# Kernel tuning notes

Hardware: AMD Instinct MI355X
Metric: run time of the kernel (lower is better)

Reference implementation:

```python
import jax
import jax.numpy as jnp
from jax import lax
import numpy as np

B, C, H, W = 16, 96, 112, 112
HIDDEN = 4 * C
LN_EPS = 1e-6  # ConvNeXt LayerNorm eps


def setup_inputs() -> dict:
    key = jax.random.key(0)
    ks = jax.random.split(key, 8)
    x = jax.random.normal(ks[0], (B, C, H, W), dtype=jnp.float32)
    # depthwise 7x7 kernel, HWIO with feature_group_count=C -> (7,7,1,C)
    dw_w = jax.random.normal(ks[1], (7, 7, 1, C), dtype=jnp.float32) * 0.02
    dw_b = jnp.zeros((C,), dtype=jnp.float32)
    gamma = jnp.ones((C,), dtype=jnp.float32)
    beta = jnp.zeros((C,), dtype=jnp.float32)
    w1 = jax.random.normal(ks[2], (C, HIDDEN), dtype=jnp.float32) * 0.02
    b1 = jnp.zeros((HIDDEN,), dtype=jnp.float32)
    w2 = jax.random.normal(ks[3], (HIDDEN, C), dtype=jnp.float32) * 0.02
    b2 = jnp.zeros((C,), dtype=jnp.float32)
    scale = jnp.full((C,), 1e-6, dtype=jnp.float32)  # block_scale init 1e-6
    return {"x": x, "dw_w": dw_w, "dw_b": dw_b, "gamma": gamma, "beta": beta,
            "w1": w1, "b1": b1, "w2": w2, "b2": b2, "scale": scale}


def reference(x, dw_w, dw_b, gamma, beta, w1, b1, w2, b2, scale):
    # depthwise 7x7, stride 1, padding 3 (SAME), groups = C
    y = lax.conv_general_dilated(
        x, dw_w, window_strides=(1, 1), padding="SAME",
        dimension_numbers=("NCHW", "HWIO", "NCHW"),
        feature_group_count=C,
    ) + dw_b[None, :, None, None]
    # BCHW -> BHWC
    y = jnp.transpose(y, (0, 2, 3, 1))
    # LayerNorm over channel dim
    mu = jnp.mean(y, axis=-1, keepdims=True)
    var = jnp.var(y, axis=-1, keepdims=True)
    y = (y - mu) * lax.rsqrt(var + LN_EPS) * gamma + beta
    # pointwise MLP with exact GELU (torch nn.GELU default)
    h = jax.nn.gelu(jnp.einsum("bhwc,cd->bhwd", y, w1) + b1, approximate=False)
    y = jnp.einsum("bhwd,dc->bhwc", h, w2) + b2
    # BHWC -> BCHW, scale, residual (eval mode: stochastic depth = identity)
    y = jnp.transpose(y, (0, 3, 1, 2))
    return scale[None, :, None, None] * y + x
```

## Files before the change

### kernel.cpp

```cpp
#include <hip/hip_runtime.h>
#include <hip/hip_bf16.h>

#define BATCH 16
#define CCH 96
#define HH 112
#define WW 112
#define HID 384
#define NPIX (BATCH * HH * WW)
#define HW (HH * WW)

#define PXB 128
#define ZROWD 50
#define SLICE_B 12288
#define RING_SLOTS 3
#define ZR_BYTES (PXB * ZROWD * 4)
#define B1_OFF (RING_SLOTS * SLICE_B)
#define SMEM_TOTAL (B1_OFF + 1536)

typedef __attribute__((ext_vector_type(8))) short bf16x8;
typedef __attribute__((ext_vector_type(4))) float f32x4;
typedef __attribute__((ext_vector_type(2))) float f32x2;
typedef __attribute__((ext_vector_type(4))) unsigned int uint4v;

typedef const __attribute__((address_space(1))) void gvoid_t;
typedef __attribute__((address_space(3))) void svoid_t;

__device__ __forceinline__ short f2bf(float v) {
    __hip_bfloat16 h = __float2bfloat16(v);
    return __builtin_bit_cast(short, h);
}
__device__ __forceinline__ float bf2f(short s) {
    unsigned int u = ((unsigned int)(unsigned short)s) << 16;
    return __builtin_bit_cast(float, u);
}
__device__ __forceinline__ float gelu_fast(float v) {
    float e = __expf(-1.702f * v);
    return v * __builtin_amdgcn_rcpf(1.0f + e);
}

__global__ __launch_bounds__(256) void pack_w(const float* __restrict__ w1,
                                              const float* __restrict__ w2,
                                              const float* __restrict__ gamma,
                                              const float* __restrict__ scale,
                                              short* __restrict__ wp) {
    int o = blockIdx.x * 256 + threadIdx.x;
    if (o >= 12 * 12 * 64 * 8) return;
    const int j   = o & 7;
    const int l   = (o >> 3) & 63;
    const int g   = o >> 9;
    const int f   = g % 12;
    const int kk2 = g / 12;
    float v;
    if (f < 6) {
        const int kk = f >> 1, mh = f & 1;
        const int c  = kk * 32 + (l >> 4) * 8 + j;
        const int d  = (2 * kk2 + mh) * 16 + (l & 15);
        v = gamma[c] * w1[c * HID + d];
    } else {
        const int nt2 = f - 6;
        const int dd  = kk2 * 32 + ((j >> 2) << 4) + ((l >> 4) << 2) + (j & 3);
        const int n   = nt2 * 16 + (l & 15);
        v = w2[dd * CCH + n] * scale[n];
    }
    wp[o] = f2bf(v);
}

__global__ __launch_bounds__(256) void pack_bias(const float* __restrict__ w1,
                                                 const float* __restrict__ b1,
                                                 const float* __restrict__ beta,
                                                 const float* __restrict__ b2,
                                                 const float* __restrict__ scale,
                                                 float* __restrict__ b1p,
                                                 float* __restrict__ b2p) {
    int t = blockIdx.x * 256 + threadIdx.x;
    if (t < HID) {
        float s = b1[t];
        for (int c = 0; c < CCH; ++c) s += beta[c] * w1[c * HID + t];
        b1p[t] = s;
    } else if (t < HID + CCH) {
        int c = t - HID;
        b2p[c] = scale[c] * b2[c];
    }
}

__global__ __launch_bounds__(256) void conv_kernel(
    const float* __restrict__ x, const float* __restrict__ dww,
    const float* __restrict__ dwb, short* __restrict__ y)
{
    __shared__ float xs[34][128];

    const int t = threadIdx.x;
    const int p = blockIdx.x;
    int o = (p & 7) * 768 + (p >> 3);
    const int ht = o & 3;  o >>= 2;
    const int c  = o % CCH;
    const int b  = o / CCH;
    const int h0 = ht * 28;
    const float* xc = x + (size_t)(b * CCH + c) * HW;

    float4 vbuf[5];
    #pragma unroll
    for (int k = 0; k < 5; ++k) {
        const int idx = t + 256 * k;
        const int r  = idx >> 5;
        const int j  = idx & 31;
        const int gh = h0 - 3 + r;
        float4 v = make_float4(0.f, 0.f, 0.f, 0.f);
        if (idx < 1088 && (unsigned)gh < HH && j >= 1 && j <= 28)
            v = *reinterpret_cast<const float4*>(xc + gh * WW + 4 * j - 4);
        vbuf[k] = v;
    }
    #pragma unroll
    for (int k = 0; k < 5; ++k) {
        const int idx = t + 256 * k;
        if (idx < 1088)
            *reinterpret_cast<float4*>(&xs[0][0] + (idx >> 5) * 128 + (idx & 31) * 4) = vbuf[k];
    }
    __syncthreads();

    const int col = t & 127;
    const int rg  = t >> 7;
    if (col < WW) {
        const int r0 = rg * 14;
        const float bias = dwb[c];
        f32x2 accp[7];
        #pragma unroll
        for (int r = 0; r < 7; ++r) accp[r] = (f32x2){bias, bias};
        #pragma unroll
        for (int kw = 0; kw < 7; ++kw) {
            float cv[20];
            #pragma unroll
            for (int i = 0; i < 20; ++i) cv[i] = xs[r0 + i][col + kw + 1];
            #pragma unroll
            for (int kh = 0; kh < 7; ++kh) {
                const float wt = dww[(kh * 7 + kw) * CCH + c];
                const f32x2 wt2 = (f32x2){wt, wt};
                #pragma unroll
                for (int r = 0; r < 7; ++r) {
                    f32x2 v;
                    v.x = cv[2 * r + kh];
                    v.y = cv[2 * r + kh + 1];
                    accp[r] += v * wt2;
                }
            }
        }
        short* yc = y + (size_t)(b * CCH + c) * HW + (h0 + r0) * WW + col;
        #pragma unroll
        for (int r = 0; r < 7; ++r) {
            yc[(2 * r) * WW]     = f2bf(accp[r].x);
            yc[(2 * r + 1) * WW] = f2bf(accp[r].y);
        }
    }
}

__global__ __launch_bounds__(256, 4) void mlp_kernel(
    const short* __restrict__ ybuf, const char* __restrict__ wp,
    const float* __restrict__ b1p, const float* __restrict__ b2p,
    const float* __restrict__ x, float* __restrict__ out)
{
    __shared__ __align__(16) char smem[SMEM_TOTAL];
    unsigned int* zr = (unsigned int*)smem;
    float* b1l = (float*)(smem + B1_OFF);

    const int t    = threadIdx.x;
    const int lane = t & 63;
    const int wv   = t >> 6;
    const int l15  = lane & 15;
    const int q    = lane >> 4;
    const int px0  = blockIdx.x * PXB;
    const int b    = px0 / HW;
    const int hw0  = px0 - b * HW;

    if (t < 192) {
        const int pq = t / 48;
        const int cp = t - pq * 48;
        const unsigned int* Ap = (const unsigned int*)(ybuf +
            (size_t)(b * CCH + 2 * cp) * HW + hw0 + pq * 32);
        const unsigned int* Bp = (const unsigned int*)(ybuf +
            (size_t)(b * CCH + 2 * cp + 1) * HW + hw0 + pq * 32);
        #pragma unroll
        for (int e = 0; e < 4; ++e) {
            const uint4v A  = *reinterpret_cast<const uint4v*>(Ap + e * 4);
            const uint4v Bv = *reinterpret_cast<const uint4v*>(Bp + e * 4);
            #pragma unroll
            for (int k = 0; k < 4; ++k) {
                const int px = pq * 32 + e * 8 + 2 * k;
                zr[px * ZROWD + cp]       = (A[k] & 0xffffu) | (Bv[k] << 16);
                zr[(px + 1) * ZROWD + cp] = (A[k] >> 16) | (Bv[k] & 0xffff0000u);
            }
        }
    } else {
        const int i0 = (t - 192) * 6;
        #pragma unroll
        for (int i2 = 0; i2 < 6; ++i2) b1l[i0 + i2] = b1p[i0 + i2];
    }

    f32x4 acc2[2][6];
    #pragma unroll
    for (int nt2 = 0; nt2 < 6; ++nt2) {
        const int c = nt2 * 16 + l15;
        const float bv = b2p[c];
        #pragma unroll
        for (int m2 = 0; m2 < 2; ++m2) {
            const size_t g = (size_t)(b * CCH + c) * HW + hw0 + wv * 32 + m2 * 16 + q * 4;
            const f32x4 xv = *reinterpret_cast<const f32x4*>(x + g);
            acc2[m2][nt2].x = bv + xv.x;  acc2[m2][nt2].y = bv + xv.y;
            acc2[m2][nt2].z = bv + xv.z;  acc2[m2][nt2].w = bv + xv.w;
        }
    }
    __syncthreads();

    bf16x8 za[2][3];
    #pragma unroll
    for (int nt = 0; nt < 2; ++nt) {
        const int row = wv * 32 + nt * 16 + l15;
        const char* base = smem + row * (ZROWD * 4) + q * 16;
        float s1 = 0.f, s2 = 0.f;
        #pragma unroll
        for (int kk = 0; kk < 3; ++kk) {
            za[nt][kk] = *reinterpret_cast<const bf16x8*>(base + kk * 64);
            #pragma unroll
            for (int j = 0; j < 8; ++j) {
                const float v = bf2f(za[nt][kk][j]);
                s1 += v; s2 += v * v;
            }
        }
        s1 += __shfl_xor(s1, 16, 64);  s2 += __shfl_xor(s2, 16, 64);
        s1 += __shfl_xor(s1, 32, 64);  s2 += __shfl_xor(s2, 32, 64);
        const float mu   = s1 * (1.0f / CCH);
        const float rstd = rsqrtf(s2 * (1.0f / CCH) - mu * mu + 1e-6f);
        #pragma unroll
        for (int kk = 0; kk < 3; ++kk)
            #pragma unroll
            for (int j = 0; j < 8; ++j)
                za[nt][kk][j] = f2bf((bf2f(za[nt][kk][j]) - mu) * rstd);
    }
    __syncthreads();

    asm volatile("s_waitcnt vmcnt(0)" ::: "memory");

    #define STAGE_F(SL, SLOT)                                                       \
        {                                                                           \
            const char* _s = wp + (size_t)(SL) * SLICE_B + (wv * 3) * 1024 +        \
                             lane * 16;                                             \
            char* _d = smem + (SLOT) * SLICE_B + (wv * 3) * 1024;                   \
            __builtin_amdgcn_global_load_lds((gvoid_t*)(_s),        (svoid_t*)(_d),        16, 0, 0); \
            __builtin_amdgcn_global_load_lds((gvoid_t*)(_s + 1024), (svoid_t*)(_d + 1024), 16, 0, 0); \
            __builtin_amdgcn_global_load_lds((gvoid_t*)(_s + 2048), (svoid_t*)(_d + 2048), 16, 0, 0); \
        }
    #define WAITBAR()                                                               \
        {                                                                           \
            asm volatile("s_waitcnt vmcnt(3)" ::: "memory");                        \
            __builtin_amdgcn_s_barrier();                                           \
            __builtin_amdgcn_sched_barrier(0);                                      \
        }

    STAGE_F(0, 0);

    #pragma unroll
    for (int kk2 = 0; kk2 < 12; ++kk2) {
        {
            const int sl = (kk2 + 1 > 11) ? 11 : kk2 + 1;
            STAGE_F(sl, sl % RING_SLOTS);
        }
        WAITBAR();
        const char* wb = smem + (kk2 % RING_SLOTS) * SLICE_B + lane * 16;

        f32x4 p0[2], p1[2];
        const f32x4 bva = *reinterpret_cast<const f32x4*>(b1l + 32 * kk2 + q * 4);
        const f32x4 bvb = *reinterpret_cast<const f32x4*>(b1l + 32 * kk2 + 16 + q * 4);
        p0[0] = bva;  p0[1] = bva;
        p1[0] = bvb;  p1[1] = bvb;
        #pragma unroll
        for (int kk = 0; kk < 3; ++kk) {
            const bf16x8 wfa = *reinterpret_cast<const bf16x8*>(wb + (kk * 2) * 1024);
            const bf16x8 wfb = *reinterpret_cast<const bf16x8*>(wb + (kk * 2 + 1) * 1024);
            p0[0] = __builtin_amdgcn_mfma_f32_16x16x32_bf16(wfa, za[0][kk], p0[0], 0, 0, 0);
            p0[1] = __builtin_amdgcn_mfma_f32_16x16x32_bf16(wfa, za[1][kk], p0[1], 0, 0, 0);
            p1[0] = __builtin_amdgcn_mfma_f32_16x16x32_bf16(wfb, za[0][kk], p1[0], 0, 0, 0);
            p1[1] = __builtin_amdgcn_mfma_f32_16x16x32_bf16(wfb, za[1][kk], p1[1], 0, 0, 0);
        }
        bf16x8 hv[2];
        #pragma unroll
        for (int nt = 0; nt < 2; ++nt)
            #pragma unroll
            for (int i = 0; i < 4; ++i) {
                hv[nt][i]     = f2bf(gelu_fast(p0[nt][i]));
                hv[nt][4 + i] = f2bf(gelu_fast(p1[nt][i]));
            }
        #pragma unroll
        for (int nt2 = 0; nt2 < 6; ++nt2) {
            const bf16x8 bfr = *reinterpret_cast<const bf16x8*>(wb + (6 + nt2) * 1024);
            acc2[0][nt2] = __builtin_amdgcn_mfma_f32_16x16x32_bf16(hv[0], bfr, acc2[0][nt2], 0, 0, 0);
            acc2[1][nt2] = __builtin_amdgcn_mfma_f32_16x16x32_bf16(hv[1], bfr, acc2[1][nt2], 0, 0, 0);
        }
    }
    #undef STAGE_F
    #undef WAITBAR

    #pragma unroll
    for (int m2 = 0; m2 < 2; ++m2) {
        const int pxl = hw0 + wv * 32 + m2 * 16 + q * 4;
        #pragma unroll
        for (int nt2 = 0; nt2 < 6; ++nt2) {
            const int c = nt2 * 16 + l15;
            const size_t g = (size_t)(b * CCH + c) * HW + pxl;
            *reinterpret_cast<f32x4*>(out + g) = acc2[m2][nt2];
        }
    }
}

extern "C" void kernel_launch(void* const* d_in, const int* in_sizes, int n_in,
                              void* d_out, int out_size, void* d_ws, size_t ws_size,
                              hipStream_t stream) {
    const float* x     = (const float*)d_in[0];
    const float* dww   = (const float*)d_in[1];
    const float* dwb   = (const float*)d_in[2];
    const float* gamma = (const float*)d_in[3];
    const float* beta  = (const float*)d_in[4];
    const float* w1    = (const float*)d_in[5];
    const float* b1    = (const float*)d_in[6];
    const float* w2    = (const float*)d_in[7];
    const float* b2    = (const float*)d_in[8];
    const float* scale = (const float*)d_in[9];
    float* out = (float*)d_out;

    char* ws = (char*)d_ws;
    short* ybuf = (short*)ws;
    const size_t Y_BYTES = (size_t)NPIX * CCH * 2;
    short* wp  = (short*)(ws + Y_BYTES);
    float* b1p = (float*)(ws + Y_BYTES + 12 * SLICE_B);
    float* b2p = b1p + HID;

    pack_w<<<(12 * 12 * 64 * 8 + 255) / 256, 256, 0, stream>>>(w1, w2, gamma, scale, wp);
    pack_bias<<<2, 256, 0, stream>>>(w1, b1, beta, b2, scale, b1p, b2p);
    conv_kernel<<<BATCH * CCH * 4, 256, 0, stream>>>(x, dww, dwb, ybuf);
    mlp_kernel<<<NPIX / PXB, 256, 0, stream>>>(ybuf, (const char*)wp, b1p, b2p, x, out);
}
```

Measured before the change: 116.2 us.

## Restructure depthwise conv to row-per-thread and shrink MLP blocks to 64 pixels

The depthwise conv now gives each thread one output row segment of 16 columns. It loads float4 quads from a padded shared tile (stride 132) and packs the bf16 outputs into two 16-byte stores instead of scalar short stores. The MLP kernel drops to 128 threads and 64 pixels per block with a two-slot weight ring, where each wave stages 6 KB per slice. It waits with vmcnt(0) before each barrier instead of the deeper three-slot prefetch. This trades pipelining depth for smaller blocks and more blocks in flight, and it changes the conv's shared-memory access pattern and register use.

```diff
diff --git a/kernel.cpp b/kernel.cpp
--- a/kernel.cpp
+++ b/kernel.cpp
@@ -9,17 +9,17 @@
 #define NPIX (BATCH * HH * WW)
 #define HW (HH * WW)
 
-#define PXB 128
+#define PXB 64
 #define ZROWD 50
 #define SLICE_B 12288
-#define RING_SLOTS 3
-#define ZR_BYTES (PXB * ZROWD * 4)
-#define B1_OFF (RING_SLOTS * SLICE_B)
-#define SMEM_TOTAL (B1_OFF + 1536)
+#define RING_B (2 * SLICE_B)
+#define B1_OFF RING_B
+#define SMEM_TOTAL (RING_B + 1536)
+
+#define XSTR 132
 
 typedef __attribute__((ext_vector_type(8))) short bf16x8;
 typedef __attribute__((ext_vector_type(4))) float f32x4;
-typedef __attribute__((ext_vector_type(2))) float f32x2;
 typedef __attribute__((ext_vector_type(4))) unsigned int uint4v;
 
 typedef const __attribute__((address_space(1))) void gvoid_t;
@@ -87,7 +87,7 @@
     const float* __restrict__ x, const float* __restrict__ dww,
     const float* __restrict__ dwb, short* __restrict__ y)
 {
-    __shared__ float xs[34][128];
+    __shared__ float xs[34 * XSTR];
 
     const int t = threadIdx.x;
     const int p = blockIdx.x;
@@ -114,46 +114,49 @@
     for (int k = 0; k < 5; ++k) {
         const int idx = t + 256 * k;
         if (idx < 1088)
-            *reinterpret_cast<float4*>(&xs[0][0] + (idx >> 5) * 128 + (idx & 31) * 4) = vbuf[k];
+            *reinterpret_cast<float4*>(&xs[(idx >> 5) * XSTR + (idx & 31) * 4]) = vbuf[k];
     }
     __syncthreads();
 
-    const int col = t & 127;
-    const int rg  = t >> 7;
-    if (col < WW) {
-        const int r0 = rg * 14;
+    const int wg = t >> 5;
+    const int r  = t & 31;
+    if (wg < 7 && r < 28) {
+        const int j0 = wg * 16;
         const float bias = dwb[c];
-        f32x2 accp[7];
-        #pragma unroll
-        for (int r = 0; r < 7; ++r) accp[r] = (f32x2){bias, bias};
-        #pragma unroll
-        for (int kw = 0; kw < 7; ++kw) {
-            float cv[20];
-            #pragma unroll
-            for (int i = 0; i < 20; ++i) cv[i] = xs[r0 + i][col + kw + 1];
-            #pragma unroll
-            for (int kh = 0; kh < 7; ++kh) {
+        float acc[16];
+        #pragma unroll
+        for (int i = 0; i < 16; ++i) acc[i] = bias;
+        #pragma unroll
+        for (int kh = 0; kh < 7; ++kh) {
+            f32x4 qd[6];
+            #pragma unroll
+            for (int u = 0; u < 6; ++u)
+                qd[u] = *reinterpret_cast<const f32x4*>(&xs[(r + kh) * XSTR + j0 + 4 * u]);
+            #pragma unroll
+            for (int kw = 0; kw < 7; ++kw) {
                 const float wt = dww[(kh * 7 + kw) * CCH + c];
-                const f32x2 wt2 = (f32x2){wt, wt};
                 #pragma unroll
-                for (int r = 0; r < 7; ++r) {
-                    f32x2 v;
-                    v.x = cv[2 * r + kh];
-                    v.y = cv[2 * r + kh + 1];
-                    accp[r] += v * wt2;
+                for (int i = 0; i < 16; ++i) {
+                    const int jj = i + kw + 1;
+                    acc[i] += qd[jj >> 2][jj & 3] * wt;
                 }
             }
         }
-        short* yc = y + (size_t)(b * CCH + c) * HW + (h0 + r0) * WW + col;
-        #pragma unroll
-        for (int r = 0; r < 7; ++r) {
-            yc[(2 * r) * WW]     = f2bf(accp[r].x);
-            yc[(2 * r + 1) * WW] = f2bf(accp[r].y);
-        }
-    }
-}
-
-__global__ __launch_bounds__(256, 4) void mlp_kernel(
+        uint4v w0, w1v;
+        #pragma unroll
+        for (int u = 0; u < 4; ++u) {
+            w0[u]  = (unsigned int)(unsigned short)f2bf(acc[2 * u]) |
+                     ((unsigned int)(unsigned short)f2bf(acc[2 * u + 1]) << 16);
+            w1v[u] = (unsigned int)(unsigned short)f2bf(acc[8 + 2 * u]) |
+                     ((unsigned int)(unsigned short)f2bf(acc[9 + 2 * u]) << 16);
+        }
+        short* yc = y + (size_t)(b * CCH + c) * HW + (h0 + r) * WW + j0;
+        *reinterpret_cast<uint4v*>(yc)     = w0;
+        *reinterpret_cast<uint4v*>(yc + 8) = w1v;
+    }
+}
+
+__global__ __launch_bounds__(128) void mlp_kernel(
     const short* __restrict__ ybuf, const char* __restrict__ wp,
     const float* __restrict__ b1p, const float* __restrict__ b2p,
     const float* __restrict__ x, float* __restrict__ out)
@@ -171,28 +174,28 @@
     const int b    = px0 / HW;
     const int hw0  = px0 - b * HW;
 
-    if (t < 192) {
-        const int pq = t / 48;
-        const int cp = t - pq * 48;
+    if (t < 96) {
+        const int pxq = t / 48;
+        const int cp  = t - pxq * 48;
         const unsigned int* Ap = (const unsigned int*)(ybuf +
-            (size_t)(b * CCH + 2 * cp) * HW + hw0 + pq * 32);
+            (size_t)(b * CCH + 2 * cp) * HW + hw0 + pxq * 32);
         const unsigned int* Bp = (const unsigned int*)(ybuf +
-            (size_t)(b * CCH + 2 * cp + 1) * HW + hw0 + pq * 32);
+            (size_t)(b * CCH + 2 * cp + 1) * HW + hw0 + pxq * 32);
         #pragma unroll
         for (int e = 0; e < 4; ++e) {
             const uint4v A  = *reinterpret_cast<const uint4v*>(Ap + e * 4);
             const uint4v Bv = *reinterpret_cast<const uint4v*>(Bp + e * 4);
             #pragma unroll
             for (int k = 0; k < 4; ++k) {
-                const int px = pq * 32 + e * 8 + 2 * k;
+                const int px = pxq * 32 + e * 8 + 2 * k;
                 zr[px * ZROWD + cp]       = (A[k] & 0xffffu) | (Bv[k] << 16);
                 zr[(px + 1) * ZROWD + cp] = (A[k] >> 16) | (Bv[k] & 0xffff0000u);
             }
         }
     } else {
-        const int i0 = (t - 192) * 6;
-        #pragma unroll
-        for (int i2 = 0; i2 < 6; ++i2) b1l[i0 + i2] = b1p[i0 + i2];
+        const int i0 = (t - 96) * 12;
+        #pragma unroll
+        for (int i2 = 0; i2 < 12; ++i2) b1l[i0 + i2] = b1p[i0 + i2];
     }
 
     f32x4 acc2[2][6];
@@ -241,30 +244,27 @@
 
     #define STAGE_F(SL, SLOT)                                                       \
         {                                                                           \
-            const char* _s = wp + (size_t)(SL) * SLICE_B + (wv * 3) * 1024 +        \
+            const char* _s = wp + (size_t)(SL) * SLICE_B + (wv * 6) * 1024 +        \
                              lane * 16;                                             \
-            char* _d = smem + (SLOT) * SLICE_B + (wv * 3) * 1024;                   \
+            char* _d = smem + (SLOT) * SLICE_B + (wv * 6) * 1024;                   \
             __builtin_amdgcn_global_load_lds((gvoid_t*)(_s),        (svoid_t*)(_d),        16, 0, 0); \
             __builtin_amdgcn_global_load_lds((gvoid_t*)(_s + 1024), (svoid_t*)(_d + 1024), 16, 0, 0); \
             __builtin_amdgcn_global_load_lds((gvoid_t*)(_s + 2048), (svoid_t*)(_d + 2048), 16, 0, 0); \
-        }
-    #define WAITBAR()                                                               \
-        {                                                                           \
-            asm volatile("s_waitcnt vmcnt(3)" ::: "memory");                        \
-            __builtin_amdgcn_s_barrier();                                           \
-            __builtin_amdgcn_sched_barrier(0);                                      \
+            __builtin_amdgcn_global_load_lds((gvoid_t*)(_s + 3072), (svoid_t*)(_d + 3072), 16, 0, 0); \
+            __builtin_amdgcn_global_load_lds((gvoid_t*)(_s + 4096), (svoid_t*)(_d + 4096), 16, 0, 0); \
+            __builtin_amdgcn_global_load_lds((gvoid_t*)(_s + 5120), (svoid_t*)(_d + 5120), 16, 0, 0); \
         }
 
     STAGE_F(0, 0);
 
     #pragma unroll
     for (int kk2 = 0; kk2 < 12; ++kk2) {
-        {
-            const int sl = (kk2 + 1 > 11) ? 11 : kk2 + 1;
-            STAGE_F(sl, sl % RING_SLOTS);
-        }
-        WAITBAR();
-        const char* wb = smem + (kk2 % RING_SLOTS) * SLICE_B + lane * 16;
+        asm volatile("s_waitcnt vmcnt(0)" ::: "memory");
+        __builtin_amdgcn_s_barrier();
+        __builtin_amdgcn_sched_barrier(0);
+        if (kk2 < 11) STAGE_F(kk2 + 1, (kk2 + 1) & 1);
+
+        const char* wb = smem + (kk2 & 1) * SLICE_B + lane * 16;
 
         f32x4 p0[2], p1[2];
         const f32x4 bva = *reinterpret_cast<const f32x4*>(b1l + 32 * kk2 + q * 4);
@@ -296,7 +296,6 @@
         }
     }
     #undef STAGE_F
-    #undef WAITBAR
 
     #pragma unroll
     for (int m2 = 0; m2 < 2; ++m2) {
@@ -335,5 +334,5 @@
     pack_w<<<(12 * 12 * 64 * 8 + 255) / 256, 256, 0, stream>>>(w1, w2, gamma, scale, wp);
     pack_bias<<<2, 256, 0, stream>>>(w1, b1, beta, b2, scale, b1p, b2p);
     conv_kernel<<<BATCH * CCH * 4, 256, 0, stream>>>(x, dww, dwb, ybuf);
-    mlp_kernel<<<NPIX / PXB, 256, 0, stream>>>(ybuf, (const char*)wp, b1p, b2p, x, out);
-}
+    mlp_kernel<<<NPIX / PXB, 128, 0, stream>>>(ybuf, (const char*)wp, b1p, b2p, x, out);
+}
```

After: 124.2 us. 6.8% more time.
